# Performance work log

Hardware: AMD Instinct MI355X
Metric: run time of the kernel (lower is better)

The kernel has to match this reference:

```python
import jax, jax.numpy as jnp
import numpy as np

B, T, D = 4, 1024, 512
E, TOP_K, H = 8, 2, 256


def setup_inputs() -> dict:
    key = jax.random.key(0)
    ks = jax.random.split(key, 8)
    s = 0.02
    return {
        "x": jax.random.normal(ks[0], (B, T, D), dtype=jnp.float32),
        "router": jax.random.normal(ks[1], (D, E), dtype=jnp.float32) * s,
        "shared_gate": jax.random.normal(ks[2], (D, H), dtype=jnp.float32) * s,
        "shared_up": jax.random.normal(ks[3], (D, H), dtype=jnp.float32) * s,
        "shared_down": jax.random.normal(ks[4], (H, D), dtype=jnp.float32) * s,
        "W_gate": jax.random.normal(ks[5], (E, D, H), dtype=jnp.float32) * s,
        "W_up": jax.random.normal(ks[6], (E, D, H), dtype=jnp.float32) * s,
        "W_down": jax.random.normal(ks[7], (E, H, D), dtype=jnp.float32) * s,
    }


def reference(x, router, shared_gate, shared_up, shared_down, W_gate, W_up, W_down):
    b, t, d = x.shape
    n = b * t
    x_flat = x.reshape(n, d)

    # shared expert (SwiGLU)
    shared_out = (jax.nn.silu(x_flat @ shared_gate) * (x_flat @ shared_up)) @ shared_down

    # router: softmax then top-k (matches torch.topk on probs)
    probs = jax.nn.softmax(x_flat @ router, axis=-1)          # [N, E]
    topk_scores, topk_idx = jax.lax.top_k(probs, TOP_K)        # [N, K]

    # dense combine weights: combine[n, e] = score if expert e chosen for token n
    combine = jnp.zeros((n, E), dtype=x.dtype)
    combine = combine.at[jnp.arange(n)[:, None], topk_idx].set(topk_scores)

    # per-expert SwiGLU over all tokens; combine masks out unrouted pairs.
    # weight multiply before down-proj in the original is linear, so folding the
    # per-token score into the combine after the down-proj is the same math.
    gate = jax.nn.silu(jnp.einsum('nd,edh->enh', x_flat, W_gate))  # [E, N, H]
    up = jnp.einsum('nd,edh->enh', x_flat, W_up)                    # [E, N, H]
    y = jnp.einsum('enh,ehd->end', gate * up, W_down)               # [E, N, D]
    routed_out = jnp.einsum('ne,end->nd', combine, y)               # [N, D]

    return (shared_out + routed_out).reshape(b, t, d)
```

## Files before the change

### kernel.cpp

```cpp
#include <hip/hip_runtime.h>
#include <hip/hip_bf16.h>
#include <math.h>

#define N_TOK 4096
#define D_DIM 512
#define E_NUM 8
#define H_DIM 256

typedef __attribute__((ext_vector_type(8))) short short8v;
typedef __attribute__((ext_vector_type(4))) float floatx4;

union U4S8 { uint4 u; short8v s; };

__device__ inline floatx4 mfma_bf16(short8v a, short8v b, floatx4 c) {
    return __builtin_amdgcn_mfma_f32_16x16x32_bf16(a, b, c, 0, 0, 0);
}

__device__ inline unsigned short f2bf(float f) {
    union { float f; unsigned u; } v; v.f = f;
    unsigned r = v.u + 0x7FFFu + ((v.u >> 16) & 1u);
    return (unsigned short)(r >> 16);
}
__device__ inline unsigned pack2(float a, float b) {
    return (unsigned)f2bf(a) | ((unsigned)f2bf(b) << 16);
}
__device__ inline void calc_offs(const int* __restrict__ counts, int* offs) {
    int a = 0;
    #pragma unroll
    for (int e = 0; e < E_NUM; e++) { offs[e] = a; a += counts[e]; }
    offs[E_NUM] = a;
}

__global__ void init_kernel(int* counts, int* nextp) {
    int t = threadIdx.x;
    if (t < 16) { counts[t] = 0; nextp[t] = 0; }
}

__global__ __launch_bounds__(256)
void router_kernel(const float* __restrict__ x, const float* __restrict__ router,
                   int* __restrict__ topk_idx, float* __restrict__ topk_sc,
                   int* __restrict__ counts) {
    __shared__ int csh[E_NUM];
    int t = threadIdx.x;
    if (t < E_NUM) csh[t] = 0;
    __syncthreads();

    int wave = t >> 6, lane = t & 63;
    float R[8][8];
    #pragma unroll
    for (int q = 0; q < 8; q++) {
        #pragma unroll
        for (int h = 0; h < 2; h++) {
            float4 v = *reinterpret_cast<const float4*>(
                router + (size_t)(lane * 8 + q) * E_NUM + h * 4);
            R[q][h * 4 + 0] = v.x; R[q][h * 4 + 1] = v.y;
            R[q][h * 4 + 2] = v.z; R[q][h * 4 + 3] = v.w;
        }
    }
    int cnt[E_NUM];
    #pragma unroll
    for (int e = 0; e < E_NUM; e++) cnt[e] = 0;

    #pragma unroll
    for (int it = 0; it < 4; it++) {
        int n = (blockIdx.x * 4 + wave) * 4 + it;
        const float* xr = x + (size_t)n * D_DIM + lane * 8;
        float4 xa = *reinterpret_cast<const float4*>(xr);
        float4 xb = *reinterpret_cast<const float4*>(xr + 4);
        float xs[8] = {xa.x, xa.y, xa.z, xa.w, xb.x, xb.y, xb.z, xb.w};

        float acc[E_NUM];
        #pragma unroll
        for (int e = 0; e < E_NUM; e++) acc[e] = 0.f;
        #pragma unroll
        for (int q = 0; q < 8; q++)
            #pragma unroll
            for (int e = 0; e < E_NUM; e++)
                acc[e] = fmaf(xs[q], R[q][e], acc[e]);
        #pragma unroll
        for (int s = 1; s < 64; s <<= 1) {
            #pragma unroll
            for (int e = 0; e < E_NUM; e++)
                acc[e] += __shfl_xor(acc[e], s);
        }
        float mx = acc[0];
        #pragma unroll
        for (int e = 1; e < E_NUM; e++) mx = fmaxf(mx, acc[e]);
        float p[E_NUM], s = 0.f;
        #pragma unroll
        for (int e = 0; e < E_NUM; e++) { p[e] = expf(acc[e] - mx); s += p[e]; }
        float inv = 1.f / s;

        int i0 = 0; float p0 = p[0];
        #pragma unroll
        for (int e = 1; e < E_NUM; e++)
            if (p[e] > p0) { p0 = p[e]; i0 = e; }
        int i1 = -1; float p1 = -1.f;
        #pragma unroll
        for (int e = 0; e < E_NUM; e++)
            if (e != i0 && p[e] > p1) { p1 = p[e]; i1 = e; }

        if (lane == 0) {
            topk_idx[n * 2 + 0] = i0;
            topk_idx[n * 2 + 1] = i1;
            topk_sc[n * 2 + 0]  = p0 * inv;
            topk_sc[n * 2 + 1]  = p1 * inv;
            #pragma unroll
            for (int e = 0; e < E_NUM; e++)
                cnt[e] += (i0 == e) + (i1 == e);
        }
    }
    if (lane == 0) {
        #pragma unroll
        for (int e = 0; e < E_NUM; e++)
            if (cnt[e]) atomicAdd(&csh[e], cnt[e]);
    }
    __syncthreads();
    if (t < E_NUM && csh[t]) atomicAdd(&counts[t], csh[t]);
}

__global__ __launch_bounds__(256)
void place_kernel(const int* __restrict__ topk_idx, const float* __restrict__ topk_sc,
                  const int* __restrict__ counts, int* __restrict__ nextp,
                  int* __restrict__ list_tok, float* __restrict__ list_sc) {
    int offs[E_NUM + 1];
    calc_offs(counts, offs);
    int n = blockIdx.x * 256 + threadIdx.x;
    int lane = threadIdx.x & 63;
    for (int k = 0; k < 2; k++) {
        int e = topk_idx[n * 2 + k];
        float sc = topk_sc[n * 2 + k];
        #pragma unroll
        for (int ee = 0; ee < E_NUM; ee++) {
            unsigned long long m = __ballot(e == ee);
            if (m == 0ull) continue;
            int leader = __ffsll((long long)m) - 1;
            int base = 0;
            if (lane == leader) base = atomicAdd(&nextp[ee], (int)__popcll(m));
            base = __shfl(base, leader);
            if (e == ee) {
                int pos = base + (int)__popcll(m & ((1ull << lane) - 1ull));
                int slot = offs[ee] + pos;
                list_tok[slot] = n;
                list_sc[slot]  = sc;
            }
        }
    }
}

__global__ __launch_bounds__(256)
void prep_frag(const float* __restrict__ Wg, const float* __restrict__ Wu,
               const float* __restrict__ shg, const float* __restrict__ shu,
               const float* __restrict__ Wd, const float* __restrict__ shd,
               unsigned short* __restrict__ WguF, unsigned short* __restrict__ WdF) {
    int wid = threadIdx.x >> 6, lane = threadIdx.x & 63;
    int job = blockIdx.x * 4 + wid;
    int kg = lane >> 4, ln = lane & 15;
    if (job < 288) {
        int e = job >> 5, r = job & 31, gu = r >> 4, nt = r & 15;
        const float* S = (e < E_NUM) ? ((gu ? Wu : Wg) + (size_t)e * 131072)
                                     : (gu ? shu : shg);
        unsigned short* D = WguF + ((size_t)((e * 2 + gu) * 16 + nt) * 16) * 512 + lane * 8;
        for (int ks = 0; ks < 16; ks++) {
            float v[8];
            #pragma unroll
            for (int j = 0; j < 8; j++)
                v[j] = S[(size_t)(ks * 32 + kg * 8 + j) * H_DIM + nt * 16 + ln];
            uint4 o;
            o.x = pack2(v[0], v[1]); o.y = pack2(v[2], v[3]);
            o.z = pack2(v[4], v[5]); o.w = pack2(v[6], v[7]);
            *reinterpret_cast<uint4*>(D + ks * 512) = o;
        }
    } else if (job < 576) {
        int j2 = job - 288;
        int e = j2 >> 5, nt = j2 & 31;
        const float* S = (e < E_NUM) ? (Wd + (size_t)e * 131072) : shd;
        unsigned short* D = WdF + ((size_t)(e * 32 + nt) * 8) * 512 + lane * 8;
        for (int ks = 0; ks < 8; ks++) {
            float v[8];
            #pragma unroll
            for (int j = 0; j < 8; j++)
                v[j] = S[(size_t)(ks * 32 + kg * 8 + j) * D_DIM + nt * 16 + ln];
            uint4 o;
            o.x = pack2(v[0], v[1]); o.y = pack2(v[2], v[3]);
            o.z = pack2(v[4], v[5]); o.w = pack2(v[6], v[7]);
            *reinterpret_cast<uint4*>(D + ks * 512) = o;
        }
    }
}

__global__ __launch_bounds__(256)
void gemm1_kernel(const float* __restrict__ x, const unsigned short* __restrict__ WguF,
                  const int* __restrict__ counts, const int* __restrict__ list_tok,
                  const float* __restrict__ list_sc,
                  unsigned short* __restrict__ H1s, unsigned short* __restrict__ H1r) {
    int ez = blockIdx.z;
    int offs[E_NUM + 1];
    calc_offs(counts, offs);
    int beg = 0, M;
    if (ez == E_NUM) { M = N_TOK; }
    else { beg = offs[ez]; M = counts[ez]; }
    int wid = threadIdx.x >> 6, lane = threadIdx.x & 63;
    int stile = blockIdx.x * 4 + wid;
    if (stile * 16 >= M) return;
    int nt0 = blockIdx.y * 4;
    int kg = lane >> 4, ln = lane & 15;

    int m_lane = stile * 16 + ln;
    int srow;
    if (ez == E_NUM) srow = m_lane;
    else srow = list_tok[beg + (m_lane < M ? m_lane : M - 1)];
    const float* ap = x + (size_t)srow * D_DIM + kg * 8;

    const unsigned short* bgp = WguF + ((size_t)((ez * 2 + 0) * 16 + nt0) * 16) * 512 + lane * 8;
    const unsigned short* bup = WguF + ((size_t)((ez * 2 + 1) * 16 + nt0) * 16) * 512 + lane * 8;

    floatx4 zf = {0.f, 0.f, 0.f, 0.f};
    floatx4 accg[4], accu[4];
    #pragma unroll
    for (int nf = 0; nf < 4; nf++) { accg[nf] = zf; accu[nf] = zf; }

    float4 aL[2], aH[2];
    uint4 vg[2][4], vu[2][4];
    aL[0] = *reinterpret_cast<const float4*>(ap);
    aH[0] = *reinterpret_cast<const float4*>(ap + 4);
    #pragma unroll
    for (int nf = 0; nf < 4; nf++) {
        vg[0][nf] = *reinterpret_cast<const uint4*>(bgp + nf * 8192);
        vu[0][nf] = *reinterpret_cast<const uint4*>(bup + nf * 8192);
    }
    #pragma unroll
    for (int ks = 0; ks < 16; ks++) {
        const int cur = ks & 1, nxt = cur ^ 1;
        if (ks < 15) {
            aL[nxt] = *reinterpret_cast<const float4*>(ap + (ks + 1) * 32);
            aH[nxt] = *reinterpret_cast<const float4*>(ap + (ks + 1) * 32 + 4);
            #pragma unroll
            for (int nf = 0; nf < 4; nf++) {
                vg[nxt][nf] = *reinterpret_cast<const uint4*>(bgp + nf * 8192 + (ks + 1) * 512);
                vu[nxt][nf] = *reinterpret_cast<const uint4*>(bup + nf * 8192 + (ks + 1) * 512);
            }
        }
        U4S8 A;
        A.u.x = pack2(aL[cur].x, aL[cur].y);
        A.u.y = pack2(aL[cur].z, aL[cur].w);
        A.u.z = pack2(aH[cur].x, aH[cur].y);
        A.u.w = pack2(aH[cur].z, aH[cur].w);
        #pragma unroll
        for (int nf = 0; nf < 4; nf++) {
            U4S8 g, u; g.u = vg[cur][nf]; u.u = vu[cur][nf];
            accg[nf] = mfma_bf16(A.s, g.s, accg[nf]);
            accu[nf] = mfma_bf16(A.s, u.s, accu[nf]);
        }
    }

    #pragma unroll
    for (int j = 0; j < 4; j++) {
        int m = stile * 16 + kg * 4 + j;
        if (m >= M) continue;
        float sc = 1.f;
        unsigned short* drow;
        if (ez == E_NUM) drow = H1s + (size_t)m * H_DIM;
        else { sc = list_sc[beg + m]; drow = H1r + (size_t)(beg + m) * H_DIM; }
        #pragma unroll
        for (int nf = 0; nf < 4; nf++) {
            float g = accg[nf][j];
            float u = accu[nf][j];
            float h = g / (1.f + expf(-g)) * u * sc;
            drow[(nt0 + nf) * 16 + ln] = f2bf(h);
        }
    }
}

__global__ __launch_bounds__(256)
void down_kernel(const unsigned short* __restrict__ H1s, const unsigned short* __restrict__ H1r,
                 const unsigned short* __restrict__ WdF, const int* __restrict__ counts,
                 const int* __restrict__ list_tok, float* __restrict__ out, int routed) {
    int beg = 0, M, eidx;
    if (routed) {
        int e = blockIdx.z;
        int offs[E_NUM + 1];
        calc_offs(counts, offs);
        beg = offs[e]; M = counts[e]; eidx = e;
    } else { M = N_TOK; eidx = E_NUM; }
    int wid = threadIdx.x >> 6, lane = threadIdx.x & 63;
    int stile = blockIdx.x * 4 + wid;
    if (stile * 16 >= M) return;
    int nt0 = blockIdx.y * 4;
    int kg = lane >> 4, ln = lane & 15;

    const unsigned short* H1 = routed ? H1r : H1s;
    const unsigned short* ap = H1 + (size_t)(beg + stile * 16 + ln) * H_DIM + kg * 8;
    const unsigned short* bp = WdF + ((size_t)(eidx * 32 + nt0) * 8) * 512 + lane * 8;

    floatx4 zf = {0.f, 0.f, 0.f, 0.f};
    floatx4 acc[4];
    #pragma unroll
    for (int nf = 0; nf < 4; nf++) acc[nf] = zf;

    uint4 av[2], bv[2][4];
    av[0] = *reinterpret_cast<const uint4*>(ap);
    #pragma unroll
    for (int nf = 0; nf < 4; nf++)
        bv[0][nf] = *reinterpret_cast<const uint4*>(bp + nf * 4096);
    #pragma unroll
    for (int ks = 0; ks < 8; ks++) {
        const int cur = ks & 1, nxt = cur ^ 1;
        if (ks < 7) {
            av[nxt] = *reinterpret_cast<const uint4*>(ap + (ks + 1) * 32);
            #pragma unroll
            for (int nf = 0; nf < 4; nf++)
                bv[nxt][nf] = *reinterpret_cast<const uint4*>(bp + nf * 4096 + (ks + 1) * 512);
        }
        U4S8 A; A.u = av[cur];
        #pragma unroll
        for (int nf = 0; nf < 4; nf++) {
            U4S8 b; b.u = bv[cur][nf];
            acc[nf] = mfma_bf16(A.s, b.s, acc[nf]);
        }
    }

    #pragma unroll
    for (int j = 0; j < 4; j++) {
        int m = stile * 16 + kg * 4 + j;
        if (m >= M) continue;
        if (!routed) {
            float* orow = out + (size_t)m * D_DIM;
            #pragma unroll
            for (int nf = 0; nf < 4; nf++)
                orow[(nt0 + nf) * 16 + ln] = acc[nf][j];
        } else {
            int tok = list_tok[beg + m];
            float* orow = out + (size_t)tok * D_DIM;
            #pragma unroll
            for (int nf = 0; nf < 4; nf++)
                atomicAdd(&orow[(nt0 + nf) * 16 + ln], acc[nf][j]);
        }
    }
}

extern "C" void kernel_launch(void* const* d_in, const int* in_sizes, int n_in,
                              void* d_out, int out_size, void* d_ws, size_t ws_size,
                              hipStream_t stream) {
    const float* x      = (const float*)d_in[0];
    const float* router = (const float*)d_in[1];
    const float* shg    = (const float*)d_in[2];
    const float* shu    = (const float*)d_in[3];
    const float* shd    = (const float*)d_in[4];
    const float* Wg     = (const float*)d_in[5];
    const float* Wu     = (const float*)d_in[6];
    const float* Wd     = (const float*)d_in[7];
    float* out = (float*)d_out;

    char* ws = (char*)d_ws;
    int*   counts   = (int*)(ws + 0);
    int*   nextp    = (int*)(ws + 64);
    int*   topk_idx = (int*)(ws + 256);
    float* topk_sc  = (float*)(ws + 256 + 1 * 32768);
    int*   list_tok = (int*)(ws + 256 + 2 * 32768);
    float* list_sc  = (float*)(ws + 256 + 3 * 32768);
    unsigned short* WguF = (unsigned short*)(ws + 256 + 4 * 32768);
    unsigned short* WdF  = WguF + (size_t)288 * 16 * 512;
    unsigned short* H1s  = WdF + (size_t)288 * 8 * 512;
    unsigned short* H1r  = H1s + (size_t)N_TOK * H_DIM;

    hipLaunchKernelGGL(init_kernel,   dim3(1),   dim3(64),  0, stream, counts, nextp);
    hipLaunchKernelGGL(router_kernel, dim3(256), dim3(256), 0, stream,
                       x, router, topk_idx, topk_sc, counts);
    hipLaunchKernelGGL(place_kernel,  dim3(16),  dim3(256), 0, stream,
                       topk_idx, topk_sc, counts, nextp, list_tok, list_sc);
    hipLaunchKernelGGL(prep_frag,     dim3(144), dim3(256), 0, stream,
                       Wg, Wu, shg, shu, Wd, shd, WguF, WdF);
    hipLaunchKernelGGL(gemm1_kernel,  dim3(64, 4, 9), dim3(256), 0, stream,
                       x, WguF, counts, list_tok, list_sc, H1s, H1r);
    hipLaunchKernelGGL(down_kernel,   dim3(64, 8, 1), dim3(256), 0, stream,
                       H1s, H1r, WdF, counts, list_tok, out, 0);
    hipLaunchKernelGGL(down_kernel,   dim3(64, 8, 8), dim3(256), 0, stream,
                       H1s, H1r, WdF, counts, list_tok, out, 1);
}
```

Measured before the change: 187.5 us.

## Widen per-wave M tile to 64 rows in gemm1 and down kernels

```diff
diff --git a/kernel.cpp b/kernel.cpp
--- a/kernel.cpp
+++ b/kernel.cpp
@@ -189,7 +189,7 @@
     }
 }
 
-__global__ __launch_bounds__(256)
+__global__ __launch_bounds__(256, 1)
 void gemm1_kernel(const float* __restrict__ x, const unsigned short* __restrict__ WguF,
                   const int* __restrict__ counts, const int* __restrict__ list_tok,
                   const float* __restrict__ list_sc,
@@ -202,28 +202,37 @@
     else { beg = offs[ez]; M = counts[ez]; }
     int wid = threadIdx.x >> 6, lane = threadIdx.x & 63;
     int stile = blockIdx.x * 4 + wid;
-    if (stile * 16 >= M) return;
+    if (stile * 64 >= M) return;
     int nt0 = blockIdx.y * 4;
     int kg = lane >> 4, ln = lane & 15;
 
-    int m_lane = stile * 16 + ln;
-    int srow;
-    if (ez == E_NUM) srow = m_lane;
-    else srow = list_tok[beg + (m_lane < M ? m_lane : M - 1)];
-    const float* ap = x + (size_t)srow * D_DIM + kg * 8;
+    const float* ap[4];
+    #pragma unroll
+    for (int rt = 0; rt < 4; rt++) {
+        int m_lane = stile * 64 + rt * 16 + ln;
+        int srow;
+        if (ez == E_NUM) srow = m_lane < M ? m_lane : M - 1;
+        else srow = list_tok[beg + (m_lane < M ? m_lane : M - 1)];
+        ap[rt] = x + (size_t)srow * D_DIM + kg * 8;
+    }
 
     const unsigned short* bgp = WguF + ((size_t)((ez * 2 + 0) * 16 + nt0) * 16) * 512 + lane * 8;
     const unsigned short* bup = WguF + ((size_t)((ez * 2 + 1) * 16 + nt0) * 16) * 512 + lane * 8;
 
     floatx4 zf = {0.f, 0.f, 0.f, 0.f};
-    floatx4 accg[4], accu[4];
-    #pragma unroll
-    for (int nf = 0; nf < 4; nf++) { accg[nf] = zf; accu[nf] = zf; }
-
-    float4 aL[2], aH[2];
+    floatx4 accg[4][4], accu[4][4];
+    #pragma unroll
+    for (int rt = 0; rt < 4; rt++)
+        #pragma unroll
+        for (int nf = 0; nf < 4; nf++) { accg[rt][nf] = zf; accu[rt][nf] = zf; }
+
+    float4 aL[2][4], aH[2][4];
     uint4 vg[2][4], vu[2][4];
-    aL[0] = *reinterpret_cast<const float4*>(ap);
-    aH[0] = *reinterpret_cast<const float4*>(ap + 4);
+    #pragma unroll
+    for (int rt = 0; rt < 4; rt++) {
+        aL[0][rt] = *reinterpret_cast<const float4*>(ap[rt]);
+        aH[0][rt] = *reinterpret_cast<const float4*>(ap[rt] + 4);
+    }
     #pragma unroll
     for (int nf = 0; nf < 4; nf++) {
         vg[0][nf] = *reinterpret_cast<const uint4*>(bgp + nf * 8192);
@@ -233,46 +242,58 @@
     for (int ks = 0; ks < 16; ks++) {
         const int cur = ks & 1, nxt = cur ^ 1;
         if (ks < 15) {
-            aL[nxt] = *reinterpret_cast<const float4*>(ap + (ks + 1) * 32);
-            aH[nxt] = *reinterpret_cast<const float4*>(ap + (ks + 1) * 32 + 4);
+            #pragma unroll
+            for (int rt = 0; rt < 4; rt++) {
+                aL[nxt][rt] = *reinterpret_cast<const float4*>(ap[rt] + (ks + 1) * 32);
+                aH[nxt][rt] = *reinterpret_cast<const float4*>(ap[rt] + (ks + 1) * 32 + 4);
+            }
             #pragma unroll
             for (int nf = 0; nf < 4; nf++) {
                 vg[nxt][nf] = *reinterpret_cast<const uint4*>(bgp + nf * 8192 + (ks + 1) * 512);
                 vu[nxt][nf] = *reinterpret_cast<const uint4*>(bup + nf * 8192 + (ks + 1) * 512);
             }
         }
-        U4S8 A;
-        A.u.x = pack2(aL[cur].x, aL[cur].y);
-        A.u.y = pack2(aL[cur].z, aL[cur].w);
-        A.u.z = pack2(aH[cur].x, aH[cur].y);
-        A.u.w = pack2(aH[cur].z, aH[cur].w);
+        U4S8 A[4];
+        #pragma unroll
+        for (int rt = 0; rt < 4; rt++) {
+            A[rt].u.x = pack2(aL[cur][rt].x, aL[cur][rt].y);
+            A[rt].u.y = pack2(aL[cur][rt].z, aL[cur][rt].w);
+            A[rt].u.z = pack2(aH[cur][rt].x, aH[cur][rt].y);
+            A[rt].u.w = pack2(aH[cur][rt].z, aH[cur][rt].w);
+        }
         #pragma unroll
         for (int nf = 0; nf < 4; nf++) {
             U4S8 g, u; g.u = vg[cur][nf]; u.u = vu[cur][nf];
-            accg[nf] = mfma_bf16(A.s, g.s, accg[nf]);
-            accu[nf] = mfma_bf16(A.s, u.s, accu[nf]);
-        }
-    }
-
-    #pragma unroll
-    for (int j = 0; j < 4; j++) {
-        int m = stile * 16 + kg * 4 + j;
-        if (m >= M) continue;
-        float sc = 1.f;
-        unsigned short* drow;
-        if (ez == E_NUM) drow = H1s + (size_t)m * H_DIM;
-        else { sc = list_sc[beg + m]; drow = H1r + (size_t)(beg + m) * H_DIM; }
-        #pragma unroll
-        for (int nf = 0; nf < 4; nf++) {
-            float g = accg[nf][j];
-            float u = accu[nf][j];
-            float h = g / (1.f + expf(-g)) * u * sc;
-            drow[(nt0 + nf) * 16 + ln] = f2bf(h);
-        }
-    }
-}
-
-__global__ __launch_bounds__(256)
+            #pragma unroll
+            for (int rt = 0; rt < 4; rt++) {
+                accg[rt][nf] = mfma_bf16(A[rt].s, g.s, accg[rt][nf]);
+                accu[rt][nf] = mfma_bf16(A[rt].s, u.s, accu[rt][nf]);
+            }
+        }
+    }
+
+    #pragma unroll
+    for (int rt = 0; rt < 4; rt++) {
+        #pragma unroll
+        for (int j = 0; j < 4; j++) {
+            int m = stile * 64 + rt * 16 + kg * 4 + j;
+            if (m >= M) continue;
+            float sc = 1.f;
+            unsigned short* drow;
+            if (ez == E_NUM) drow = H1s + (size_t)m * H_DIM;
+            else { sc = list_sc[beg + m]; drow = H1r + (size_t)(beg + m) * H_DIM; }
+            #pragma unroll
+            for (int nf = 0; nf < 4; nf++) {
+                float g = accg[rt][nf][j];
+                float u = accu[rt][nf][j];
+                float h = g / (1.f + expf(-g)) * u * sc;
+                drow[(nt0 + nf) * 16 + ln] = f2bf(h);
+            }
+        }
+    }
+}
+
+__global__ __launch_bounds__(256, 1)
 void down_kernel(const unsigned short* __restrict__ H1s, const unsigned short* __restrict__ H1r,
                  const unsigned short* __restrict__ WdF, const int* __restrict__ counts,
                  const int* __restrict__ list_tok, float* __restrict__ out, int routed) {
@@ -285,21 +306,31 @@
     } else { M = N_TOK; eidx = E_NUM; }
     int wid = threadIdx.x >> 6, lane = threadIdx.x & 63;
     int stile = blockIdx.x * 4 + wid;
-    if (stile * 16 >= M) return;
+    if (stile * 64 >= M) return;
     int nt0 = blockIdx.y * 4;
     int kg = lane >> 4, ln = lane & 15;
 
     const unsigned short* H1 = routed ? H1r : H1s;
-    const unsigned short* ap = H1 + (size_t)(beg + stile * 16 + ln) * H_DIM + kg * 8;
+    const unsigned short* ap[4];
+    #pragma unroll
+    for (int rt = 0; rt < 4; rt++) {
+        int m_lane = stile * 64 + rt * 16 + ln;
+        int idx = m_lane < M ? m_lane : M - 1;
+        ap[rt] = H1 + (size_t)(beg + idx) * H_DIM + kg * 8;
+    }
     const unsigned short* bp = WdF + ((size_t)(eidx * 32 + nt0) * 8) * 512 + lane * 8;
 
     floatx4 zf = {0.f, 0.f, 0.f, 0.f};
-    floatx4 acc[4];
-    #pragma unroll
-    for (int nf = 0; nf < 4; nf++) acc[nf] = zf;
-
-    uint4 av[2], bv[2][4];
-    av[0] = *reinterpret_cast<const uint4*>(ap);
+    floatx4 acc[4][4];
+    #pragma unroll
+    for (int rt = 0; rt < 4; rt++)
+        #pragma unroll
+        for (int nf = 0; nf < 4; nf++) acc[rt][nf] = zf;
+
+    uint4 av[2][4], bv[2][4];
+    #pragma unroll
+    for (int rt = 0; rt < 4; rt++)
+        av[0][rt] = *reinterpret_cast<const uint4*>(ap[rt]);
     #pragma unroll
     for (int nf = 0; nf < 4; nf++)
         bv[0][nf] = *reinterpret_cast<const uint4*>(bp + nf * 4096);
@@ -307,34 +338,42 @@
     for (int ks = 0; ks < 8; ks++) {
         const int cur = ks & 1, nxt = cur ^ 1;
         if (ks < 7) {
-            av[nxt] = *reinterpret_cast<const uint4*>(ap + (ks + 1) * 32);
+            #pragma unroll
+            for (int rt = 0; rt < 4; rt++)
+                av[nxt][rt] = *reinterpret_cast<const uint4*>(ap[rt] + (ks + 1) * 32);
             #pragma unroll
             for (int nf = 0; nf < 4; nf++)
                 bv[nxt][nf] = *reinterpret_cast<const uint4*>(bp + nf * 4096 + (ks + 1) * 512);
         }
-        U4S8 A; A.u = av[cur];
         #pragma unroll
         for (int nf = 0; nf < 4; nf++) {
             U4S8 b; b.u = bv[cur][nf];
-            acc[nf] = mfma_bf16(A.s, b.s, acc[nf]);
-        }
-    }
-
-    #pragma unroll
-    for (int j = 0; j < 4; j++) {
-        int m = stile * 16 + kg * 4 + j;
-        if (m >= M) continue;
-        if (!routed) {
-            float* orow = out + (size_t)m * D_DIM;
-            #pragma unroll
-            for (int nf = 0; nf < 4; nf++)
-                orow[(nt0 + nf) * 16 + ln] = acc[nf][j];
-        } else {
-            int tok = list_tok[beg + m];
-            float* orow = out + (size_t)tok * D_DIM;
-            #pragma unroll
-            for (int nf = 0; nf < 4; nf++)
-                atomicAdd(&orow[(nt0 + nf) * 16 + ln], acc[nf][j]);
+            #pragma unroll
+            for (int rt = 0; rt < 4; rt++) {
+                U4S8 A; A.u = av[cur][rt];
+                acc[rt][nf] = mfma_bf16(A.s, b.s, acc[rt][nf]);
+            }
+        }
+    }
+
+    #pragma unroll
+    for (int rt = 0; rt < 4; rt++) {
+        #pragma unroll
+        for (int j = 0; j < 4; j++) {
+            int m = stile * 64 + rt * 16 + kg * 4 + j;
+            if (m >= M) continue;
+            if (!routed) {
+                float* orow = out + (size_t)m * D_DIM;
+                #pragma unroll
+                for (int nf = 0; nf < 4; nf++)
+                    orow[(nt0 + nf) * 16 + ln] = acc[rt][nf][j];
+            } else {
+                int tok = list_tok[beg + m];
+                float* orow = out + (size_t)tok * D_DIM;
+                #pragma unroll
+                for (int nf = 0; nf < 4; nf++)
+                    atomicAdd(&orow[(nt0 + nf) * 16 + ln], acc[rt][nf][j]);
+            }
         }
     }
 }
@@ -371,10 +410,10 @@
                        topk_idx, topk_sc, counts, nextp, list_tok, list_sc);
     hipLaunchKernelGGL(prep_frag,     dim3(144), dim3(256), 0, stream,
                        Wg, Wu, shg, shu, Wd, shd, WguF, WdF);
-    hipLaunchKernelGGL(gemm1_kernel,  dim3(64, 4, 9), dim3(256), 0, stream,
+    hipLaunchKernelGGL(gemm1_kernel,  dim3(16, 4, 9), dim3(256), 0, stream,
                        x, WguF, counts, list_tok, list_sc, H1s, H1r);
-    hipLaunchKernelGGL(down_kernel,   dim3(64, 8, 1), dim3(256), 0, stream,
+    hipLaunchKernelGGL(down_kernel,   dim3(16, 8, 1), dim3(256), 0, stream,
                        H1s, H1r, WdF, counts, list_tok, out, 0);
-    hipLaunchKernelGGL(down_kernel,   dim3(64, 8, 8), dim3(256), 0, stream,
+    hipLaunchKernelGGL(down_kernel,   dim3(16, 8, 8), dim3(256), 0, stream,
                        H1s, H1r, WdF, counts, list_tok, out, 1);
 }
```

Result: slower. 289.0 us (+54.1%).

## Pre-convert x to bf16 in router, parallelize weight prep, deepen gemm prefetch

Applied to the files above, without the earlier changes.

```diff
diff --git a/kernel.cpp b/kernel.cpp
--- a/kernel.cpp
+++ b/kernel.cpp
@@ -39,7 +39,7 @@
 __global__ __launch_bounds__(256)
 void router_kernel(const float* __restrict__ x, const float* __restrict__ router,
                    int* __restrict__ topk_idx, float* __restrict__ topk_sc,
-                   int* __restrict__ counts) {
+                   int* __restrict__ counts, unsigned short* __restrict__ xb) {
     __shared__ int csh[E_NUM];
     int t = threadIdx.x;
     if (t < E_NUM) csh[t] = 0;
@@ -66,8 +66,13 @@
         int n = (blockIdx.x * 4 + wave) * 4 + it;
         const float* xr = x + (size_t)n * D_DIM + lane * 8;
         float4 xa = *reinterpret_cast<const float4*>(xr);
-        float4 xb = *reinterpret_cast<const float4*>(xr + 4);
-        float xs[8] = {xa.x, xa.y, xa.z, xa.w, xb.x, xb.y, xb.z, xb.w};
+        float4 xb4 = *reinterpret_cast<const float4*>(xr + 4);
+        float xs[8] = {xa.x, xa.y, xa.z, xa.w, xb4.x, xb4.y, xb4.z, xb4.w};
+
+        uint4 xo;
+        xo.x = pack2(xs[0], xs[1]); xo.y = pack2(xs[2], xs[3]);
+        xo.z = pack2(xs[4], xs[5]); xo.w = pack2(xs[6], xs[7]);
+        *reinterpret_cast<uint4*>(xb + (size_t)n * D_DIM + lane * 8) = xo;
 
         float acc[E_NUM];
         #pragma unroll
@@ -156,41 +161,39 @@
     int wid = threadIdx.x >> 6, lane = threadIdx.x & 63;
     int job = blockIdx.x * 4 + wid;
     int kg = lane >> 4, ln = lane & 15;
-    if (job < 288) {
-        int e = job >> 5, r = job & 31, gu = r >> 4, nt = r & 15;
+    if (job < 4608) {
+        int panel = job >> 4, ks = job & 15;
+        int e = panel >> 5, r = panel & 31, gu = r >> 4, nt = r & 15;
         const float* S = (e < E_NUM) ? ((gu ? Wu : Wg) + (size_t)e * 131072)
                                      : (gu ? shu : shg);
-        unsigned short* D = WguF + ((size_t)((e * 2 + gu) * 16 + nt) * 16) * 512 + lane * 8;
-        for (int ks = 0; ks < 16; ks++) {
-            float v[8];
-            #pragma unroll
-            for (int j = 0; j < 8; j++)
-                v[j] = S[(size_t)(ks * 32 + kg * 8 + j) * H_DIM + nt * 16 + ln];
-            uint4 o;
-            o.x = pack2(v[0], v[1]); o.y = pack2(v[2], v[3]);
-            o.z = pack2(v[4], v[5]); o.w = pack2(v[6], v[7]);
-            *reinterpret_cast<uint4*>(D + ks * 512) = o;
-        }
-    } else if (job < 576) {
-        int j2 = job - 288;
-        int e = j2 >> 5, nt = j2 & 31;
+        unsigned short* D = WguF + ((size_t)((e * 2 + gu) * 16 + nt) * 16 + ks) * 512 + lane * 8;
+        float v[8];
+        #pragma unroll
+        for (int j = 0; j < 8; j++)
+            v[j] = S[(size_t)(ks * 32 + kg * 8 + j) * H_DIM + nt * 16 + ln];
+        uint4 o;
+        o.x = pack2(v[0], v[1]); o.y = pack2(v[2], v[3]);
+        o.z = pack2(v[4], v[5]); o.w = pack2(v[6], v[7]);
+        *reinterpret_cast<uint4*>(D) = o;
+    } else if (job < 6912) {
+        int j2 = job - 4608;
+        int panel = j2 >> 3, ks = j2 & 7;
+        int e = panel >> 5, nt = panel & 31;
         const float* S = (e < E_NUM) ? (Wd + (size_t)e * 131072) : shd;
-        unsigned short* D = WdF + ((size_t)(e * 32 + nt) * 8) * 512 + lane * 8;
-        for (int ks = 0; ks < 8; ks++) {
-            float v[8];
-            #pragma unroll
-            for (int j = 0; j < 8; j++)
-                v[j] = S[(size_t)(ks * 32 + kg * 8 + j) * D_DIM + nt * 16 + ln];
-            uint4 o;
-            o.x = pack2(v[0], v[1]); o.y = pack2(v[2], v[3]);
-            o.z = pack2(v[4], v[5]); o.w = pack2(v[6], v[7]);
-            *reinterpret_cast<uint4*>(D + ks * 512) = o;
-        }
-    }
-}
-
-__global__ __launch_bounds__(256)
-void gemm1_kernel(const float* __restrict__ x, const unsigned short* __restrict__ WguF,
+        unsigned short* D = WdF + ((size_t)(e * 32 + nt) * 8 + ks) * 512 + lane * 8;
+        float v[8];
+        #pragma unroll
+        for (int j = 0; j < 8; j++)
+            v[j] = S[(size_t)(ks * 32 + kg * 8 + j) * D_DIM + nt * 16 + ln];
+        uint4 o;
+        o.x = pack2(v[0], v[1]); o.y = pack2(v[2], v[3]);
+        o.z = pack2(v[4], v[5]); o.w = pack2(v[6], v[7]);
+        *reinterpret_cast<uint4*>(D) = o;
+    }
+}
+
+__global__ __launch_bounds__(256)
+void gemm1_kernel(const unsigned short* __restrict__ xb, const unsigned short* __restrict__ WguF,
                   const int* __restrict__ counts, const int* __restrict__ list_tok,
                   const float* __restrict__ list_sc,
                   unsigned short* __restrict__ H1s, unsigned short* __restrict__ H1r) {
@@ -210,7 +213,7 @@
     int srow;
     if (ez == E_NUM) srow = m_lane;
     else srow = list_tok[beg + (m_lane < M ? m_lane : M - 1)];
-    const float* ap = x + (size_t)srow * D_DIM + kg * 8;
+    const unsigned short* ap = xb + (size_t)srow * D_DIM + kg * 8;
 
     const unsigned short* bgp = WguF + ((size_t)((ez * 2 + 0) * 16 + nt0) * 16) * 512 + lane * 8;
     const unsigned short* bup = WguF + ((size_t)((ez * 2 + 1) * 16 + nt0) * 16) * 512 + lane * 8;
@@ -220,32 +223,30 @@
     #pragma unroll
     for (int nf = 0; nf < 4; nf++) { accg[nf] = zf; accu[nf] = zf; }
 
-    float4 aL[2], aH[2];
-    uint4 vg[2][4], vu[2][4];
-    aL[0] = *reinterpret_cast<const float4*>(ap);
-    aH[0] = *reinterpret_cast<const float4*>(ap + 4);
-    #pragma unroll
-    for (int nf = 0; nf < 4; nf++) {
-        vg[0][nf] = *reinterpret_cast<const uint4*>(bgp + nf * 8192);
-        vu[0][nf] = *reinterpret_cast<const uint4*>(bup + nf * 8192);
+    uint4 aB[3];
+    uint4 vg[3][4], vu[3][4];
+    #pragma unroll
+    for (int pk = 0; pk < 2; pk++) {
+        aB[pk] = *reinterpret_cast<const uint4*>(ap + pk * 32);
+        #pragma unroll
+        for (int nf = 0; nf < 4; nf++) {
+            vg[pk][nf] = *reinterpret_cast<const uint4*>(bgp + nf * 8192 + pk * 512);
+            vu[pk][nf] = *reinterpret_cast<const uint4*>(bup + nf * 8192 + pk * 512);
+        }
     }
     #pragma unroll
     for (int ks = 0; ks < 16; ks++) {
-        const int cur = ks & 1, nxt = cur ^ 1;
-        if (ks < 15) {
-            aL[nxt] = *reinterpret_cast<const float4*>(ap + (ks + 1) * 32);
-            aH[nxt] = *reinterpret_cast<const float4*>(ap + (ks + 1) * 32 + 4);
+        const int cur = ks % 3;
+        if (ks + 2 < 16) {
+            const int pf = (ks + 2) % 3;
+            aB[pf] = *reinterpret_cast<const uint4*>(ap + (ks + 2) * 32);
             #pragma unroll
             for (int nf = 0; nf < 4; nf++) {
-                vg[nxt][nf] = *reinterpret_cast<const uint4*>(bgp + nf * 8192 + (ks + 1) * 512);
-                vu[nxt][nf] = *reinterpret_cast<const uint4*>(bup + nf * 8192 + (ks + 1) * 512);
+                vg[pf][nf] = *reinterpret_cast<const uint4*>(bgp + nf * 8192 + (ks + 2) * 512);
+                vu[pf][nf] = *reinterpret_cast<const uint4*>(bup + nf * 8192 + (ks + 2) * 512);
             }
         }
-        U4S8 A;
-        A.u.x = pack2(aL[cur].x, aL[cur].y);
-        A.u.y = pack2(aL[cur].z, aL[cur].w);
-        A.u.z = pack2(aH[cur].x, aH[cur].y);
-        A.u.w = pack2(aH[cur].z, aH[cur].w);
+        U4S8 A; A.u = aB[cur];
         #pragma unroll
         for (int nf = 0; nf < 4; nf++) {
             U4S8 g, u; g.u = vg[cur][nf]; u.u = vu[cur][nf];
@@ -290,7 +291,8 @@
     int kg = lane >> 4, ln = lane & 15;
 
     const unsigned short* H1 = routed ? H1r : H1s;
-    const unsigned short* ap = H1 + (size_t)(beg + stile * 16 + ln) * H_DIM + kg * 8;
+    int m_lane = stile * 16 + ln;
+    const unsigned short* ap = H1 + (size_t)(beg + (m_lane < M ? m_lane : M - 1)) * H_DIM + kg * 8;
     const unsigned short* bp = WdF + ((size_t)(eidx * 32 + nt0) * 8) * 512 + lane * 8;
 
     floatx4 zf = {0.f, 0.f, 0.f, 0.f};
@@ -298,21 +300,25 @@
     #pragma unroll
     for (int nf = 0; nf < 4; nf++) acc[nf] = zf;
 
-    uint4 av[2], bv[2][4];
-    av[0] = *reinterpret_cast<const uint4*>(ap);
-    #pragma unroll
-    for (int nf = 0; nf < 4; nf++)
-        bv[0][nf] = *reinterpret_cast<const uint4*>(bp + nf * 4096);
+    uint4 aB[3], bv[3][4];
+    #pragma unroll
+    for (int pk = 0; pk < 2; pk++) {
+        aB[pk] = *reinterpret_cast<const uint4*>(ap + pk * 32);
+        #pragma unroll
+        for (int nf = 0; nf < 4; nf++)
+            bv[pk][nf] = *reinterpret_cast<const uint4*>(bp + nf * 4096 + pk * 512);
+    }
     #pragma unroll
     for (int ks = 0; ks < 8; ks++) {
-        const int cur = ks & 1, nxt = cur ^ 1;
-        if (ks < 7) {
-            av[nxt] = *reinterpret_cast<const uint4*>(ap + (ks + 1) * 32);
+        const int cur = ks % 3;
+        if (ks + 2 < 8) {
+            const int pf = (ks + 2) % 3;
+            aB[pf] = *reinterpret_cast<const uint4*>(ap + (ks + 2) * 32);
             #pragma unroll
             for (int nf = 0; nf < 4; nf++)
-                bv[nxt][nf] = *reinterpret_cast<const uint4*>(bp + nf * 4096 + (ks + 1) * 512);
-        }
-        U4S8 A; A.u = av[cur];
+                bv[pf][nf] = *reinterpret_cast<const uint4*>(bp + nf * 4096 + (ks + 2) * 512);
+        }
+        U4S8 A; A.u = aB[cur];
         #pragma unroll
         for (int nf = 0; nf < 4; nf++) {
             U4S8 b; b.u = bv[cur][nf];
@@ -363,16 +369,17 @@
     unsigned short* WdF  = WguF + (size_t)288 * 16 * 512;
     unsigned short* H1s  = WdF + (size_t)288 * 8 * 512;
     unsigned short* H1r  = H1s + (size_t)N_TOK * H_DIM;
-
-    hipLaunchKernelGGL(init_kernel,   dim3(1),   dim3(64),  0, stream, counts, nextp);
-    hipLaunchKernelGGL(router_kernel, dim3(256), dim3(256), 0, stream,
-                       x, router, topk_idx, topk_sc, counts);
-    hipLaunchKernelGGL(place_kernel,  dim3(16),  dim3(256), 0, stream,
+    unsigned short* xb   = H1r + (size_t)2 * N_TOK * H_DIM;
+
+    hipLaunchKernelGGL(init_kernel,   dim3(1),    dim3(64),  0, stream, counts, nextp);
+    hipLaunchKernelGGL(router_kernel, dim3(256),  dim3(256), 0, stream,
+                       x, router, topk_idx, topk_sc, counts, xb);
+    hipLaunchKernelGGL(place_kernel,  dim3(16),   dim3(256), 0, stream,
                        topk_idx, topk_sc, counts, nextp, list_tok, list_sc);
-    hipLaunchKernelGGL(prep_frag,     dim3(144), dim3(256), 0, stream,
+    hipLaunchKernelGGL(prep_frag,     dim3(1728), dim3(256), 0, stream,
                        Wg, Wu, shg, shu, Wd, shd, WguF, WdF);
     hipLaunchKernelGGL(gemm1_kernel,  dim3(64, 4, 9), dim3(256), 0, stream,
-                       x, WguF, counts, list_tok, list_sc, H1s, H1r);
+                       xb, WguF, counts, list_tok, list_sc, H1s, H1r);
     hipLaunchKernelGGL(down_kernel,   dim3(64, 8, 1), dim3(256), 0, stream,
                        H1s, H1r, WdF, counts, list_tok, out, 0);
     hipLaunchKernelGGL(down_kernel,   dim3(64, 8, 8), dim3(256), 0, stream,
```

Result: faster. 180.9 us (-3.5%).
